# Kernel optimization log

Hardware: AMD Instinct MI355X
Metric: run time of the kernel (lower is better)

The kernel has to match this reference:

```python
import jax, jax.numpy as jnp
import numpy as np
from jax import lax

KS = 7  # kernel-prediction footprint at 1/4 res
DN = ('NCHW', 'OIHW', 'NCHW')


def _conv(x, W, b):
    y = lax.conv_general_dilated(x, W, (1, 1), 'VALID', dimension_numbers=DN)
    return y + b[None, :, None, None]


def _apply_kernels(kernel, data, ks):
    # kernel: [bs, ks*ks, kh, kw]; data: [bs, 1, h, w]
    kh, kw = kernel.shape[2], kernel.shape[3]
    h, w = data.shape[2], data.shape[3]
    ch = (h - (kh + ks - 1)) // 2
    cw = (w - (kw + ks - 1)) // 2
    if ch > 0:
        data = data[:, :, ch:h - ch, :]
    if cw > 0:
        data = data[:, :, :, cw:w - cw]
    # patches: [bs, ks*ks, kh, kw], flat tap index = dy*ks+dx (row-major), same as torch unfold+view
    patches = lax.conv_general_dilated_patches(data, (ks, ks), (1, 1), 'VALID')
    return jnp.sum(kernel * patches, axis=1, keepdims=True)


def _crop_like(a, b):
    dh = (a.shape[2] - b.shape[2]) // 2
    dw = (a.shape[3] - b.shape[3]) // 2
    if dh > 0 or dw > 0:
        a = a[:, :, dh:a.shape[2] - dh, dw:a.shape[3] - dw]
    return a


def _unroll(buf):
    # [bs,4,h,w] quarter-res -> [bs,1,2h,2w] full-res (channel c=2p+q -> offset (p,q))
    bs, _, h, w = buf.shape
    return buf.reshape(bs, 2, 2, h, w).transpose(0, 3, 1, 4, 2).reshape(bs, 1, 2 * h, 2 * w)


def reference(mosaic, W0, b0, W1, b1, W2, b2, W3, b3, W4, b4):
    gray = mosaic.sum(axis=1)  # [bs,H,W]
    # GRBG 2x2 phase extraction, matching torch unfold(2,2,2).unfold(1,2,2).permute(0,3,4,1,2)
    g0 = gray[:, 0::2, 0::2][:, None]
    b_ = gray[:, 1::2, 0::2][:, None]
    r = gray[:, 0::2, 1::2][:, None]
    g1 = gray[:, 1::2, 1::2][:, None]
    x = jnp.concatenate([g0, b_, r, g1], axis=1)  # [bs,4,h,w]

    # ConvChain: 5 valid 3x3 convs, relu on all but last (linear output)
    for (W, bb) in ((W0, b0), (W1, b1), (W2, b2), (W3, b3)):
        x = jax.nn.relu(_conv(x, W, bb))
    kernels = _conv(x, W4, b4)  # [bs, 10*KS*KS, kh, kw]

    k2 = KS * KS
    idx = 0

    reds = [r]
    for _ in range(3):
        k = jax.nn.softmax(kernels[:, idx:idx + k2], axis=1)
        idx += k2
        reds.append(_apply_kernels(k, r, KS))
    reds[0] = _crop_like(reds[0], reds[1])
    red = _unroll(jnp.concatenate([reds[1], reds[0], reds[2], reds[3]], axis=1))

    blues = [b_]
    for _ in range(3):
        k = jax.nn.softmax(kernels[:, idx:idx + k2], axis=1)
        idx += k2
        blues.append(_apply_kernels(k, b_, KS))
    blues[0] = _crop_like(blues[0], blues[1])
    blue = _unroll(jnp.concatenate([blues[1], blues[2], blues[0], blues[3]], axis=1))

    greens = [g0, g1]
    for _ in range(2):
        k = jax.nn.softmax(kernels[:, idx:idx + 2 * k2], axis=1)
        idx += 2 * k2
        greens.append(_apply_kernels(k[:, :k2], g0, KS) + _apply_kernels(k[:, k2:], g1, KS))
    greens[0] = _crop_like(greens[0], greens[2])
    greens[1] = _crop_like(greens[1], greens[2])
    green = _unroll(jnp.concatenate([greens[0], greens[2], greens[3], greens[1]], axis=1))

    return jnp.concatenate([red, green, blue], axis=1)  # [bs,3,2*kh,2*kw]


def setup_inputs() -> dict:
    key = jax.random.key(0)
    ks = jax.random.split(key, 6)
    bs, H, W = 2, 768, 768
    mosaic = jax.random.uniform(ks[0], (bs, 3, H, W), dtype=jnp.float32)

    def w(k, o, i):
        return jax.random.normal(k, (o, i, 3, 3), jnp.float32) * (1.0 / np.sqrt(i * 9))

    z = lambda n: jnp.zeros((n,), jnp.float32)
    return {
        'mosaic': mosaic,
        'W0': w(ks[1], 64, 4), 'b0': z(64),
        'W1': w(ks[2], 64, 64), 'b1': z(64),
        'W2': w(ks[3], 64, 64), 'b2': z(64),
        'W3': w(ks[4], 64, 64), 'b3': z(64),
        'W4': w(ks[5], 490, 64), 'b4': z(490),
    }
```

## Files before the change

### kernel.cpp

```cpp
#include <hip/hip_runtime.h>
#include <hip/hip_bf16.h>
#include <math.h>


typedef __attribute__((ext_vector_type(8))) short short8;
typedef __attribute__((ext_vector_type(4))) short short4v;
typedef __attribute__((ext_vector_type(4))) float f32x4;

static __device__ __forceinline__ short f2bf(float v) {
    __bf16 h = (__bf16)v;
    return __builtin_bit_cast(short, h);
}

__global__ __launch_bounds__(256) void split_k(const float* __restrict__ mosaic,
                                               float* __restrict__ x0) {
    int idx = blockIdx.x * 256 + threadIdx.x;
    const int total = 2 * 4 * 384 * 384;
    if (idx >= total) return;
    int x = idx % 384;
    int t = idx / 384;
    int y = t % 384;  t /= 384;
    int c = t % 4;
    int b = t / 4;
    int Y = 2 * y + ((c == 1 || c == 3) ? 1 : 0);
    int X = 2 * x + ((c == 2 || c == 3) ? 1 : 0);
    const float* mb = mosaic + (size_t)b * 3 * 768 * 768;
    float g = mb[Y * 768 + X] + mb[768 * 768 + Y * 768 + X] + mb[2 * 768 * 768 + Y * 768 + X];
    x0[idx] = g;
}

__global__ __launch_bounds__(256) void repack_k(const float* __restrict__ W,
                                                short* __restrict__ dst) {
    int idx = blockIdx.x * 256 + threadIdx.x;
    if (idx >= 9 * 64 * 64) return;
    int ic = idx % 64;
    int t2 = idx / 64;
    int oc = t2 % 64;
    int t  = t2 / 64;
    dst[idx] = f2bf(W[((size_t)oc * 64 + ic) * 9 + t]);
}

__global__ __launch_bounds__(256) void repack4_k(const float* __restrict__ W4,
                                                 const float* __restrict__ b4,
                                                 short* __restrict__ Wq,
                                                 float* __restrict__ bq) {
    int idx = blockIdx.x * 256 + threadIdx.x;
    if (idx < 9 * 640 * 64) {
        int ic  = idx % 64;
        int t2  = idx / 64;
        int ocn = t2 % 640;
        int tap = t2 / 640;
        int k  = ocn >> 6;
        int ql = ocn & 63;
        float v = (ql < 49) ? W4[((size_t)(49 * k + ql) * 64 + ic) * 9 + tap] : 0.f;
        Wq[idx] = f2bf(v);
    }
    if (idx < 640) {
        int k = idx >> 6, ql = idx & 63;
        bq[idx] = (ql < 49) ? b4[49 * k + ql] : 0.f;
    }
}

__global__ __launch_bounds__(256) void conv0_k(const float* __restrict__ x0f,
                                               const float* __restrict__ W0,
                                               const float* __restrict__ b0,
                                               short* __restrict__ out) {
    __shared__ float w[64 * 36];
    __shared__ float bb[64];
    for (int e = threadIdx.x; e < 64 * 36; e += 256) w[e] = W0[e];
    if (threadIdx.x < 64) bb[threadIdx.x] = b0[threadIdx.x];
    __syncthreads();
    int idx = blockIdx.x * 256 + threadIdx.x;
    if (idx >= 2 * 382 * 382) return;
    int x = idx % 382;
    int t = idx / 382;
    int y = t % 382;
    int b = t / 382;
    const float* base = x0f + (size_t)b * 4 * 384 * 384;
    float in[4][9];
#pragma unroll
    for (int ic = 0; ic < 4; ++ic)
#pragma unroll
        for (int ky = 0; ky < 3; ++ky)
#pragma unroll
            for (int kx = 0; kx < 3; ++kx)
                in[ic][ky * 3 + kx] = base[ic * 384 * 384 + (y + ky) * 384 + (x + kx)];
    short* op = out + (((size_t)b * 382 + y) * 382 + x) * 64;
    float accs[8];
    for (int og = 0; og < 8; ++og) {
#pragma unroll
        for (int oo = 0; oo < 8; ++oo) {
            int oc = og * 8 + oo;
            float acc = bb[oc];
            const float* wp = w + oc * 36;
#pragma unroll
            for (int ic = 0; ic < 4; ++ic)
#pragma unroll
                for (int e = 0; e < 9; ++e)
                    acc = fmaf(in[ic][e], wp[ic * 9 + e], acc);
            accs[oo] = fmaxf(acc, 0.f);
        }
        short8 pk;
#pragma unroll
        for (int oo = 0; oo < 8; ++oo) pk[oo] = f2bf(accs[oo]);
        *(short8*)(op + og * 8) = pk;
    }
}

__global__ __launch_bounds__(256) void convmfma_k(
    const short* __restrict__ act, int Hin, int Win,
    const short* __restrict__ Wq, const float* __restrict__ bias,
    short* __restrict__ out) {
    const int Wout = Win - 2;
    const int b   = blockIdx.z;
    const int y   = blockIdx.y;
    const int x0  = blockIdx.x * 64;
    const int tid  = threadIdx.x;
    const int wave = tid >> 6;
    const int lane = tid & 63;
    const int wr = wave >> 1, wc = wave & 1;

    __shared__ __align__(16) short At[64][72];
    __shared__ __align__(16) short Bt[64][72];

    const int srow = tid >> 2;
    const int sq   = tid & 3;

    short8 ra0, ra1, rb0, rb1;
    auto loadA = [&](int tap) {
        const short* p = Wq + ((size_t)tap * 64 + srow) * 64 + sq * 16;
        ra0 = *(const short8*)p;
        ra1 = *(const short8*)(p + 8);
    };
    auto loadB = [&](int tap) {
        int ky = tap / 3, kx = tap % 3;
        int xe = x0 + srow;
        if (xe > Wout - 1) xe = Wout - 1;
        xe += kx;
        const short* p = act + (((size_t)b * Hin + (y + ky)) * (size_t)Win + xe) * 64 + sq * 16;
        rb0 = *(const short8*)p;
        rb1 = *(const short8*)(p + 8);
    };

    f32x4 acc[2][2] = {};
    loadA(0);
    loadB(0);
#pragma unroll 1
    for (int tap = 0; tap < 9; ++tap) {
        if (tap) __syncthreads();
        *(short8*)&At[srow][sq * 16]     = ra0;
        *(short8*)&At[srow][sq * 16 + 8] = ra1;
        *(short8*)&Bt[srow][sq * 16]     = rb0;
        *(short8*)&Bt[srow][sq * 16 + 8] = rb1;
        __syncthreads();
        if (tap < 8) { loadA(tap + 1); loadB(tap + 1); }
        short8 af[2][2], bf[2][2];
#pragma unroll
        for (int kk = 0; kk < 2; ++kk) {
            int ic = kk * 32 + (lane >> 4) * 8;
#pragma unroll
            for (int m = 0; m < 2; ++m)
                af[kk][m] = *(const short8*)&At[wr * 32 + m * 16 + (lane & 15)][ic];
#pragma unroll
            for (int n = 0; n < 2; ++n)
                bf[kk][n] = *(const short8*)&Bt[wc * 32 + n * 16 + (lane & 15)][ic];
        }
#pragma unroll
        for (int kk = 0; kk < 2; ++kk)
#pragma unroll
            for (int m = 0; m < 2; ++m)
#pragma unroll
                for (int n = 0; n < 2; ++n)
                    acc[m][n] = __builtin_amdgcn_mfma_f32_16x16x32_bf16(
                        af[kk][m], bf[kk][n], acc[m][n], 0, 0, 0);
    }

#pragma unroll
    for (int m = 0; m < 2; ++m) {
        int ocb = wr * 32 + m * 16 + (lane >> 4) * 4;
#pragma unroll
        for (int n = 0; n < 2; ++n) {
            int x = x0 + wc * 32 + n * 16 + (lane & 15);
            if (x >= Wout) continue;
            size_t off = (((size_t)b * Wout + y) * Wout + x) * 64 + ocb;
            short4v pk;
#pragma unroll
            for (int r = 0; r < 4; ++r)
                pk[r] = f2bf(fmaxf(acc[m][n][r] + bias[ocb + r], 0.f));
            *(short4v*)(out + off) = pk;
        }
    }
}

__global__ __launch_bounds__(256) void conv4epi_k(
    const short* __restrict__ act,
    const short* __restrict__ Wq,
    const float* __restrict__ bias,
    const float* __restrict__ x0f,
    float* __restrict__ out) {
    const int Hin = 376, Win = 376, Wout = 374;
    const int z5 = blockIdx.z;
    const int b = z5 / 5;
    const int z = z5 % 5;
    const int y = blockIdx.y;
    const int x0c = blockIdx.x * 64;
    const int tid = threadIdx.x;
    const int wave = tid >> 6;
    const int lane = tid & 63;
    const int wr = wave >> 1, wc = wave & 1;
    const int l15 = lane & 15, l4 = lane >> 4;

    __shared__ __align__(16) short At[128][72];
    __shared__ __align__(16) short Bt[64][72];
    __shared__ float smM[2][64], smD[2][64], smN[2][64];

    const int arow = tid >> 1;
    const int ah   = tid & 1;
    const int brow = tid >> 2;
    const int bq   = tid & 3;

    short8 ra0, ra1, ra2, ra3, rb0, rb1;
    auto loadA = [&](int tap) {
        const short* p = Wq + ((size_t)tap * 640 + z * 128 + arow) * 64 + ah * 32;
        ra0 = *(const short8*)p;
        ra1 = *(const short8*)(p + 8);
        ra2 = *(const short8*)(p + 16);
        ra3 = *(const short8*)(p + 24);
    };
    auto loadB = [&](int tap) {
        int ky = tap / 3, kx = tap % 3;
        int xe = x0c + brow;
        if (xe > Wout - 1) xe = Wout - 1;
        xe += kx;
        const short* p = act + (((size_t)b * Hin + (y + ky)) * (size_t)Win + xe) * 64 + bq * 16;
        rb0 = *(const short8*)p;
        rb1 = *(const short8*)(p + 8);
    };

    f32x4 acc[4][2] = {};
    loadA(0);
    loadB(0);
#pragma unroll 1
    for (int tap = 0; tap < 9; ++tap) {
        if (tap) __syncthreads();
        *(short8*)&At[arow][ah * 32]      = ra0;
        *(short8*)&At[arow][ah * 32 + 8]  = ra1;
        *(short8*)&At[arow][ah * 32 + 16] = ra2;
        *(short8*)&At[arow][ah * 32 + 24] = ra3;
        *(short8*)&Bt[brow][bq * 16]      = rb0;
        *(short8*)&Bt[brow][bq * 16 + 8]  = rb1;
        __syncthreads();
        if (tap < 8) { loadA(tap + 1); loadB(tap + 1); }
        short8 af[2][4], bf[2][2];
#pragma unroll
        for (int kk = 0; kk < 2; ++kk) {
            int ic = kk * 32 + l4 * 8;
#pragma unroll
            for (int m = 0; m < 4; ++m)
                af[kk][m] = *(const short8*)&At[wr * 64 + m * 16 + l15][ic];
#pragma unroll
            for (int n = 0; n < 2; ++n)
                bf[kk][n] = *(const short8*)&Bt[wc * 32 + n * 16 + l15][ic];
        }
#pragma unroll
        for (int kk = 0; kk < 2; ++kk)
#pragma unroll
            for (int m = 0; m < 4; ++m)
#pragma unroll
                for (int n = 0; n < 2; ++n)
                    acc[m][n] = __builtin_amdgcn_mfma_f32_16x16x32_bf16(
                        af[kk][m], bf[kk][n], acc[m][n], 0, 0, 0);
    }

    const float* pb = x0f + (size_t)b * 4 * 384 * 384;
    int pidx;
    switch (z) {
        case 0: pidx = 2; break;
        case 1: pidx = wr ? 1 : 2; break;
        case 2: pidx = 1; break;
        default: pidx = wr ? 3 : 0; break;
    }
    const float* plane = pb + (size_t)pidx * 384 * 384;

    float bv[4][4];
#pragma unroll
    for (int m = 0; m < 4; ++m)
#pragma unroll
        for (int r = 0; r < 4; ++r)
            bv[m][r] = bias[z * 128 + wr * 64 + m * 16 + l4 * 4 + r];

#pragma unroll
    for (int n = 0; n < 2; ++n) {
        const int xn = x0c + wc * 32 + n * 16 + l15;
        const int xg = (xn < Wout) ? xn : (Wout - 1);
        float mx = -1e30f;
#pragma unroll
        for (int m = 0; m < 4; ++m)
#pragma unroll
            for (int r = 0; r < 4; ++r) {
                int q = m * 16 + l4 * 4 + r;
                if (q < 49) mx = fmaxf(mx, acc[m][n][r] + bv[m][r]);
            }
        mx = fmaxf(mx, __shfl_xor(mx, 16));
        mx = fmaxf(mx, __shfl_xor(mx, 32));
        float den = 0.f, num = 0.f;
#pragma unroll
        for (int m = 0; m < 4; ++m)
#pragma unroll
            for (int r = 0; r < 4; ++r) {
                int q = m * 16 + l4 * 4 + r;
                if (q < 49) {
                    float e = __expf(acc[m][n][r] + bv[m][r] - mx);
                    den += e;
                    float g = plane[(y + 2 + q / 7) * 384 + (xg + 2 + q % 7)];
                    num = fmaf(e, g, num);
                }
            }
        den += __shfl_xor(den, 16);  den += __shfl_xor(den, 32);
        num += __shfl_xor(num, 16);  num += __shfl_xor(num, 32);
        if (l4 == 0) {
            int p = wc * 32 + n * 16 + l15;
            smM[wr][p] = mx;
            smD[wr][p] = den;
            smN[wr][p] = num;
        }
    }
    __syncthreads();

    if (z < 3) {
        if (tid < 128) {
            int sub = tid >> 6, p = tid & 63;
            int x = x0c + p;
            if (x < Wout) {
                float val = smN[sub][p] / smD[sub][p];
                int t = z * 2 + sub;
                int color = (t < 3) ? 0 : 2;
                int oy, ox;
                switch (t) {
                    case 0: oy = 0; ox = 0; break;
                    case 1: oy = 1; ox = 0; break;
                    case 2: oy = 1; ox = 1; break;
                    case 3: oy = 0; ox = 0; break;
                    case 4: oy = 0; ox = 1; break;
                    default: oy = 1; ox = 1; break;
                }
                out[(((size_t)b * 3 + color) * 748 + 2 * y + oy) * 748 + 2 * x + ox] = val;
            }
        }
    } else {
        if (tid < 64) {
            int p = tid, x = x0c + p;
            if (x < Wout) {
                float m0 = smM[0][p], m1 = smM[1][p];
                float M = fmaxf(m0, m1);
                float s0 = __expf(m0 - M), s1 = __expf(m1 - M);
                float val = (smN[0][p] * s0 + smN[1][p] * s1) /
                            (smD[0][p] * s0 + smD[1][p] * s1);
                int oy = (z == 3) ? 0 : 1;
                int ox = (z == 3) ? 1 : 0;
                out[(((size_t)b * 3 + 1) * 748 + 2 * y + oy) * 748 + 2 * x + ox] = val;
            }
        }
    }
}

__global__ __launch_bounds__(256) void raw_k(const float* __restrict__ x0f,
                                             float* __restrict__ out) {
    int idx = blockIdx.x * 256 + threadIdx.x;
    if (idx >= 2 * 374 * 374) return;
    int x = idx % 374;
    int t = idx / 374;
    int y = t % 374;
    int b = t / 374;
    const float* pb = x0f + (size_t)b * 4 * 384 * 384;
    float g0v = pb[(y + 5) * 384 + x + 5];
    float blv = pb[384 * 384 + (y + 5) * 384 + x + 5];
    float rrv = pb[2 * 384 * 384 + (y + 5) * 384 + x + 5];
    float g1v = pb[3 * 384 * 384 + (y + 5) * 384 + x + 5];
    float* ob = out + (size_t)b * 3 * 748 * 748;
    ob[((size_t)0 * 748 + 2 * y) * 748 + 2 * x + 1]     = rrv;
    ob[((size_t)2 * 748 + 2 * y + 1) * 748 + 2 * x]     = blv;
    ob[((size_t)1 * 748 + 2 * y) * 748 + 2 * x]         = g0v;
    ob[((size_t)1 * 748 + 2 * y + 1) * 748 + 2 * x + 1] = g1v;
}

extern "C" void kernel_launch(void* const* d_in, const int* in_sizes, int n_in,
                              void* d_out, int out_size, void* d_ws, size_t ws_size,
                              hipStream_t stream) {
    const float* mosaic = (const float*)d_in[0];
    const float* W0 = (const float*)d_in[1];  const float* b0 = (const float*)d_in[2];
    const float* W1 = (const float*)d_in[3];  const float* b1 = (const float*)d_in[4];
    const float* W2 = (const float*)d_in[5];  const float* b2 = (const float*)d_in[6];
    const float* W3 = (const float*)d_in[7];  const float* b3 = (const float*)d_in[8];
    const float* W4 = (const float*)d_in[9];  const float* b4 = (const float*)d_in[10];
    float* out = (float*)d_out;

    char* ws = (char*)d_ws;
    float* x0f    = (float*)ws;  ws += 4718592;
    short* Wq1    = (short*)ws;  ws += 73728;
    short* Wq2    = (short*)ws;  ws += 73728;
    short* Wq3    = (short*)ws;  ws += 73728;
    short* Wq4p   = (short*)ws;  ws += 737280;
    float* bias4p = (float*)ws;  ws += 2560;
    short* bufA   = (short*)ws;  ws += 37356544;
    short* bufB   = (short*)ws;

    split_k<<<(2 * 4 * 384 * 384 + 255) / 256, 256, 0, stream>>>(mosaic, x0f);

    repack_k<<<(9 * 64 * 64 + 255) / 256, 256, 0, stream>>>(W1, Wq1);
    repack_k<<<(9 * 64 * 64 + 255) / 256, 256, 0, stream>>>(W2, Wq2);
    repack_k<<<(9 * 64 * 64 + 255) / 256, 256, 0, stream>>>(W3, Wq3);
    repack4_k<<<(9 * 640 * 64 + 255) / 256, 256, 0, stream>>>(W4, b4, Wq4p, bias4p);

    conv0_k<<<(2 * 382 * 382 + 255) / 256, 256, 0, stream>>>(x0f, W0, b0, bufA);

    convmfma_k<<<dim3(6, 380, 2), 256, 0, stream>>>(bufA, 382, 382, Wq1, b1, bufB);
    convmfma_k<<<dim3(6, 378, 2), 256, 0, stream>>>(bufB, 380, 380, Wq2, b2, bufA);
    convmfma_k<<<dim3(6, 376, 2), 256, 0, stream>>>(bufA, 378, 378, Wq3, b3, bufB);

    conv4epi_k<<<dim3(6, 374, 2 * 5), 256, 0, stream>>>(bufB, Wq4p, bias4p, x0f, out);
    raw_k<<<(2 * 374 * 374 + 255) / 256, 256, 0, stream>>>(x0f, out);
}
```

Before: 511.3 us.

## Unify convs into one templated kernel with async LDS patch staging and direct weight loads

Replaces the per-tap staged conv kernels with one templated kernel. It loads the whole 3x66 input patch into LDS once using global_load_lds, with an XOR swizzle to avoid bank conflicts. Each of the 9 taps then reads shifted slices from that patch, and weight fragments are read directly from global memory instead of being staged through LDS. The block index is remapped across 8 groups (XCD-style), which changes which blocks run together. This removes the per-tap barriers and redundant activation loads, at the cost of larger LDS use and weight reads that depend on cache hits.

```diff
diff --git a/kernel.cpp b/kernel.cpp
--- a/kernel.cpp
+++ b/kernel.cpp
@@ -107,258 +107,188 @@
     }
 }
 
-__global__ __launch_bounds__(256) void convmfma_k(
-    const short* __restrict__ act, int Hin, int Win,
-    const short* __restrict__ Wq, const float* __restrict__ bias,
-    short* __restrict__ out) {
-    const int Wout = Win - 2;
-    const int b   = blockIdx.z;
-    const int y   = blockIdx.y;
-    const int x0  = blockIdx.x * 64;
-    const int tid  = threadIdx.x;
-    const int wave = tid >> 6;
-    const int lane = tid & 63;
-    const int wr = wave >> 1, wc = wave & 1;
-
-    __shared__ __align__(16) short At[64][72];
-    __shared__ __align__(16) short Bt[64][72];
-
-    const int srow = tid >> 2;
-    const int sq   = tid & 3;
-
-    short8 ra0, ra1, rb0, rb1;
-    auto loadA = [&](int tap) {
-        const short* p = Wq + ((size_t)tap * 64 + srow) * 64 + sq * 16;
-        ra0 = *(const short8*)p;
-        ra1 = *(const short8*)(p + 8);
-    };
-    auto loadB = [&](int tap) {
-        int ky = tap / 3, kx = tap % 3;
-        int xe = x0 + srow;
-        if (xe > Wout - 1) xe = Wout - 1;
-        xe += kx;
-        const short* p = act + (((size_t)b * Hin + (y + ky)) * (size_t)Win + xe) * 64 + sq * 16;
-        rb0 = *(const short8*)p;
-        rb1 = *(const short8*)(p + 8);
-    };
-
-    f32x4 acc[2][2] = {};
-    loadA(0);
-    loadB(0);
-#pragma unroll 1
-    for (int tap = 0; tap < 9; ++tap) {
-        if (tap) __syncthreads();
-        *(short8*)&At[srow][sq * 16]     = ra0;
-        *(short8*)&At[srow][sq * 16 + 8] = ra1;
-        *(short8*)&Bt[srow][sq * 16]     = rb0;
-        *(short8*)&Bt[srow][sq * 16 + 8] = rb1;
-        __syncthreads();
-        if (tap < 8) { loadA(tap + 1); loadB(tap + 1); }
-        short8 af[2][2], bf[2][2];
-#pragma unroll
-        for (int kk = 0; kk < 2; ++kk) {
-            int ic = kk * 32 + (lane >> 4) * 8;
-#pragma unroll
-            for (int m = 0; m < 2; ++m)
-                af[kk][m] = *(const short8*)&At[wr * 32 + m * 16 + (lane & 15)][ic];
-#pragma unroll
-            for (int n = 0; n < 2; ++n)
-                bf[kk][n] = *(const short8*)&Bt[wc * 32 + n * 16 + (lane & 15)][ic];
-        }
-#pragma unroll
-        for (int kk = 0; kk < 2; ++kk)
-#pragma unroll
-            for (int m = 0; m < 2; ++m)
-#pragma unroll
-                for (int n = 0; n < 2; ++n)
-                    acc[m][n] = __builtin_amdgcn_mfma_f32_16x16x32_bf16(
-                        af[kk][m], bf[kk][n], acc[m][n], 0, 0, 0);
-    }
-
-#pragma unroll
-    for (int m = 0; m < 2; ++m) {
-        int ocb = wr * 32 + m * 16 + (lane >> 4) * 4;
-#pragma unroll
-        for (int n = 0; n < 2; ++n) {
-            int x = x0 + wc * 32 + n * 16 + (lane & 15);
-            if (x >= Wout) continue;
-            size_t off = (((size_t)b * Wout + y) * Wout + x) * 64 + ocb;
-            short4v pk;
-#pragma unroll
-            for (int r = 0; r < 4; ++r)
-                pk[r] = f2bf(fmaxf(acc[m][n][r] + bias[ocb + r], 0.f));
-            *(short4v*)(out + off) = pk;
-        }
-    }
-}
-
-__global__ __launch_bounds__(256) void conv4epi_k(
+template <int MW, bool EPI>
+__global__ __launch_bounds__(256) void convfused_k(
     const short* __restrict__ act,
+    int Hin, int Hout,
     const short* __restrict__ Wq,
+    int CoutT,
     const float* __restrict__ bias,
+    short* __restrict__ outbf,
     const float* __restrict__ x0f,
     float* __restrict__ out) {
-    const int Hin = 376, Win = 376, Wout = 374;
-    const int z5 = blockIdx.z;
-    const int b = z5 / 5;
-    const int z = z5 % 5;
-    const int y = blockIdx.y;
-    const int x0c = blockIdx.x * 64;
+    const int Win = Hin;
+    const int Wout = Hin - 2;
     const int tid = threadIdx.x;
     const int wave = tid >> 6;
     const int lane = tid & 63;
     const int wr = wave >> 1, wc = wave & 1;
     const int l15 = lane & 15, l4 = lane >> 4;
 
-    __shared__ __align__(16) short At[128][72];
-    __shared__ __align__(16) short Bt[64][72];
-    __shared__ float smM[2][64], smD[2][64], smN[2][64];
-
-    const int arow = tid >> 1;
-    const int ah   = tid & 1;
-    const int brow = tid >> 2;
-    const int bq   = tid & 3;
-
-    short8 ra0, ra1, ra2, ra3, rb0, rb1;
-    auto loadA = [&](int tap) {
-        const short* p = Wq + ((size_t)tap * 640 + z * 128 + arow) * 64 + ah * 32;
-        ra0 = *(const short8*)p;
-        ra1 = *(const short8*)(p + 8);
-        ra2 = *(const short8*)(p + 16);
-        ra3 = *(const short8*)(p + 24);
-    };
-    auto loadB = [&](int tap) {
-        int ky = tap / 3, kx = tap % 3;
-        int xe = x0c + brow;
-        if (xe > Wout - 1) xe = Wout - 1;
-        xe += kx;
-        const short* p = act + (((size_t)b * Hin + (y + ky)) * (size_t)Win + xe) * 64 + bq * 16;
-        rb0 = *(const short8*)p;
-        rb1 = *(const short8*)(p + 8);
-    };
-
-    f32x4 acc[4][2] = {};
-    loadA(0);
-    loadB(0);
-#pragma unroll 1
+    const int q8 = gridDim.x >> 3;
+    const int L = (blockIdx.x & 7) * q8 + (blockIdx.x >> 3);
+    int b, y, x0c, z;
+    if (EPI) {
+        int zx = L % 30; z = zx % 5; x0c = (zx / 5) * 64;
+        int t = L / 30;  y = t % 374; b = t / 374;
+    } else {
+        x0c = (L % 6) * 64;
+        int t = L / 6;   y = t % Hout; b = t / Hout; z = 0;
+    }
+
+    __shared__ __align__(16) short Bt[1792 * 8];
+    for (int i = 0; i < 7; ++i) {
+        int s  = i * 256 + tid;
+        int ss = s < 1584 ? s : 1583;
+        int row = ss >> 3, sl = ss & 7;
+        int ky = row / 66, xl = row % 66;
+        int gx = x0c + xl;
+        if (gx > Win - 1) gx = Win - 1;
+        const short* src = act + (((size_t)b * Hin + (y + ky)) * (size_t)Win + gx) * 64
+                               + ((sl ^ (xl & 7)) << 3);
+        __builtin_amdgcn_global_load_lds((const __attribute__((address_space(1))) void*)src,
+                                         (__attribute__((address_space(3))) void*)((char*)Bt + s * 16),
+                                         16, 0, 0);
+    }
+    __syncthreads();
+
+    const int zrow = EPI ? z * 128 : 0;
+    f32x4 acc[MW][2] = {};
+#pragma unroll
     for (int tap = 0; tap < 9; ++tap) {
-        if (tap) __syncthreads();
-        *(short8*)&At[arow][ah * 32]      = ra0;
-        *(short8*)&At[arow][ah * 32 + 8]  = ra1;
-        *(short8*)&At[arow][ah * 32 + 16] = ra2;
-        *(short8*)&At[arow][ah * 32 + 24] = ra3;
-        *(short8*)&Bt[brow][bq * 16]      = rb0;
-        *(short8*)&Bt[brow][bq * 16 + 8]  = rb1;
-        __syncthreads();
-        if (tap < 8) { loadA(tap + 1); loadB(tap + 1); }
-        short8 af[2][4], bf[2][2];
-#pragma unroll
-        for (int kk = 0; kk < 2; ++kk) {
-            int ic = kk * 32 + l4 * 8;
-#pragma unroll
-            for (int m = 0; m < 4; ++m)
-                af[kk][m] = *(const short8*)&At[wr * 64 + m * 16 + l15][ic];
-#pragma unroll
-            for (int n = 0; n < 2; ++n)
-                bf[kk][n] = *(const short8*)&Bt[wc * 32 + n * 16 + l15][ic];
-        }
+        const int ky = tap / 3, kx = tap % 3;
+        short8 af[2][MW], bf[2][2];
 #pragma unroll
         for (int kk = 0; kk < 2; ++kk)
 #pragma unroll
-            for (int m = 0; m < 4; ++m)
+            for (int m = 0; m < MW; ++m)
+                af[kk][m] = *(const short8*)(Wq +
+                    ((size_t)tap * CoutT + zrow + wr * (MW * 16) + m * 16 + l15) * 64
+                    + kk * 32 + l4 * 8);
+#pragma unroll
+        for (int kk = 0; kk < 2; ++kk)
+#pragma unroll
+            for (int n = 0; n < 2; ++n) {
+                int xl = wc * 32 + n * 16 + l15 + kx;
+                int slot = (kk * 4 + l4) ^ (xl & 7);
+                bf[kk][n] = *(const short8*)&Bt[(((ky * 66 + xl) << 3) + slot) << 3];
+            }
+#pragma unroll
+        for (int kk = 0; kk < 2; ++kk)
+#pragma unroll
+            for (int m = 0; m < MW; ++m)
 #pragma unroll
                 for (int n = 0; n < 2; ++n)
                     acc[m][n] = __builtin_amdgcn_mfma_f32_16x16x32_bf16(
                         af[kk][m], bf[kk][n], acc[m][n], 0, 0, 0);
     }
 
-    const float* pb = x0f + (size_t)b * 4 * 384 * 384;
-    int pidx;
-    switch (z) {
-        case 0: pidx = 2; break;
-        case 1: pidx = wr ? 1 : 2; break;
-        case 2: pidx = 1; break;
-        default: pidx = wr ? 3 : 0; break;
-    }
-    const float* plane = pb + (size_t)pidx * 384 * 384;
-
-    float bv[4][4];
-#pragma unroll
-    for (int m = 0; m < 4; ++m)
-#pragma unroll
-        for (int r = 0; r < 4; ++r)
-            bv[m][r] = bias[z * 128 + wr * 64 + m * 16 + l4 * 4 + r];
-
-#pragma unroll
-    for (int n = 0; n < 2; ++n) {
-        const int xn = x0c + wc * 32 + n * 16 + l15;
-        const int xg = (xn < Wout) ? xn : (Wout - 1);
-        float mx = -1e30f;
-#pragma unroll
-        for (int m = 0; m < 4; ++m)
-#pragma unroll
-            for (int r = 0; r < 4; ++r) {
-                int q = m * 16 + l4 * 4 + r;
-                if (q < 49) mx = fmaxf(mx, acc[m][n][r] + bv[m][r]);
-            }
-        mx = fmaxf(mx, __shfl_xor(mx, 16));
-        mx = fmaxf(mx, __shfl_xor(mx, 32));
-        float den = 0.f, num = 0.f;
-#pragma unroll
-        for (int m = 0; m < 4; ++m)
-#pragma unroll
-            for (int r = 0; r < 4; ++r) {
-                int q = m * 16 + l4 * 4 + r;
-                if (q < 49) {
-                    float e = __expf(acc[m][n][r] + bv[m][r] - mx);
-                    den += e;
-                    float g = plane[(y + 2 + q / 7) * 384 + (xg + 2 + q % 7)];
-                    num = fmaf(e, g, num);
+    if (!EPI) {
+#pragma unroll
+        for (int m = 0; m < MW; ++m) {
+            int ocb = wr * (MW * 16) + m * 16 + l4 * 4;
+#pragma unroll
+            for (int n = 0; n < 2; ++n) {
+                int x = x0c + wc * 32 + n * 16 + l15;
+                if (x >= Wout) continue;
+                size_t off = (((size_t)b * Wout + y) * Wout + x) * 64 + ocb;
+                short4v pk;
+#pragma unroll
+                for (int r = 0; r < 4; ++r)
+                    pk[r] = f2bf(fmaxf(acc[m][n][r] + bias[ocb + r], 0.f));
+                *(short4v*)(outbf + off) = pk;
+            }
+        }
+    } else {
+        __shared__ float smM[2][64], smD[2][64], smN[2][64];
+        const float* pb = x0f + (size_t)b * 4 * 384 * 384;
+        int pidx;
+        switch (z) {
+            case 0: pidx = 2; break;
+            case 1: pidx = wr ? 1 : 2; break;
+            case 2: pidx = 1; break;
+            default: pidx = wr ? 3 : 0; break;
+        }
+        const float* plane = pb + (size_t)pidx * 384 * 384;
+
+        float bv[MW][4];
+#pragma unroll
+        for (int m = 0; m < MW; ++m)
+#pragma unroll
+            for (int r = 0; r < 4; ++r)
+                bv[m][r] = bias[z * 128 + wr * 64 + m * 16 + l4 * 4 + r];
+
+#pragma unroll
+        for (int n = 0; n < 2; ++n) {
+            const int xn = x0c + wc * 32 + n * 16 + l15;
+            const int xg = (xn < 374) ? xn : 373;
+            float mx = -1e30f;
+#pragma unroll
+            for (int m = 0; m < MW; ++m)
+#pragma unroll
+                for (int r = 0; r < 4; ++r) {
+                    int qq = m * 16 + l4 * 4 + r;
+                    if (qq < 49) mx = fmaxf(mx, acc[m][n][r] + bv[m][r]);
                 }
-            }
-        den += __shfl_xor(den, 16);  den += __shfl_xor(den, 32);
-        num += __shfl_xor(num, 16);  num += __shfl_xor(num, 32);
-        if (l4 == 0) {
-            int p = wc * 32 + n * 16 + l15;
-            smM[wr][p] = mx;
-            smD[wr][p] = den;
-            smN[wr][p] = num;
-        }
-    }
-    __syncthreads();
-
-    if (z < 3) {
-        if (tid < 128) {
-            int sub = tid >> 6, p = tid & 63;
-            int x = x0c + p;
-            if (x < Wout) {
-                float val = smN[sub][p] / smD[sub][p];
-                int t = z * 2 + sub;
-                int color = (t < 3) ? 0 : 2;
-                int oy, ox;
-                switch (t) {
-                    case 0: oy = 0; ox = 0; break;
-                    case 1: oy = 1; ox = 0; break;
-                    case 2: oy = 1; ox = 1; break;
-                    case 3: oy = 0; ox = 0; break;
-                    case 4: oy = 0; ox = 1; break;
-                    default: oy = 1; ox = 1; break;
+            mx = fmaxf(mx, __shfl_xor(mx, 16));
+            mx = fmaxf(mx, __shfl_xor(mx, 32));
+            float den = 0.f, num = 0.f;
+#pragma unroll
+            for (int m = 0; m < MW; ++m)
+#pragma unroll
+                for (int r = 0; r < 4; ++r) {
+                    int qq = m * 16 + l4 * 4 + r;
+                    if (qq < 49) {
+                        float e = __expf(acc[m][n][r] + bv[m][r] - mx);
+                        den += e;
+                        float g = plane[(y + 2 + qq / 7) * 384 + (xg + 2 + qq % 7)];
+                        num = fmaf(e, g, num);
+                    }
                 }
-                out[(((size_t)b * 3 + color) * 748 + 2 * y + oy) * 748 + 2 * x + ox] = val;
-            }
-        }
-    } else {
-        if (tid < 64) {
-            int p = tid, x = x0c + p;
-            if (x < Wout) {
-                float m0 = smM[0][p], m1 = smM[1][p];
-                float M = fmaxf(m0, m1);
-                float s0 = __expf(m0 - M), s1 = __expf(m1 - M);
-                float val = (smN[0][p] * s0 + smN[1][p] * s1) /
-                            (smD[0][p] * s0 + smD[1][p] * s1);
-                int oy = (z == 3) ? 0 : 1;
-                int ox = (z == 3) ? 1 : 0;
-                out[(((size_t)b * 3 + 1) * 748 + 2 * y + oy) * 748 + 2 * x + ox] = val;
+            den += __shfl_xor(den, 16);  den += __shfl_xor(den, 32);
+            num += __shfl_xor(num, 16);  num += __shfl_xor(num, 32);
+            if (l4 == 0) {
+                int p = wc * 32 + n * 16 + l15;
+                smM[wr][p] = mx;
+                smD[wr][p] = den;
+                smN[wr][p] = num;
+            }
+        }
+        __syncthreads();
+
+        if (z < 3) {
+            if (tid < 128) {
+                int sub = tid >> 6, p = tid & 63;
+                int x = x0c + p;
+                if (x < 374) {
+                    float val = smN[sub][p] / smD[sub][p];
+                    int t = z * 2 + sub;
+                    int color = (t < 3) ? 0 : 2;
+                    int oy, ox;
+                    switch (t) {
+                        case 0: oy = 0; ox = 0; break;
+                        case 1: oy = 1; ox = 0; break;
+                        case 2: oy = 1; ox = 1; break;
+                        case 3: oy = 0; ox = 0; break;
+                        case 4: oy = 0; ox = 1; break;
+                        default: oy = 1; ox = 1; break;
+                    }
+                    out[(((size_t)b * 3 + color) * 748 + 2 * y + oy) * 748 + 2 * x + ox] = val;
+                }
+            }
+        } else {
+            if (tid < 64) {
+                int p = tid, x = x0c + p;
+                if (x < 374) {
+                    float m0 = smM[0][p], m1 = smM[1][p];
+                    float M = fmaxf(m0, m1);
+                    float s0 = __expf(m0 - M), s1 = __expf(m1 - M);
+                    float val = (smN[0][p] * s0 + smN[1][p] * s1) /
+                                (smD[0][p] * s0 + smD[1][p] * s1);
+                    int oy = (z == 3) ? 0 : 1;
+                    int ox = (z == 3) ? 1 : 0;
+                    out[(((size_t)b * 3 + 1) * 748 + 2 * y + oy) * 748 + 2 * x + ox] = val;
+                }
             }
         }
     }
@@ -414,10 +344,15 @@
 
     conv0_k<<<(2 * 382 * 382 + 255) / 256, 256, 0, stream>>>(x0f, W0, b0, bufA);
 
-    convmfma_k<<<dim3(6, 380, 2), 256, 0, stream>>>(bufA, 382, 382, Wq1, b1, bufB);
-    convmfma_k<<<dim3(6, 378, 2), 256, 0, stream>>>(bufB, 380, 380, Wq2, b2, bufA);
-    convmfma_k<<<dim3(6, 376, 2), 256, 0, stream>>>(bufA, 378, 378, Wq3, b3, bufB);
-
-    conv4epi_k<<<dim3(6, 374, 2 * 5), 256, 0, stream>>>(bufB, Wq4p, bias4p, x0f, out);
+    convfused_k<2, false><<<6 * 380 * 2, 256, 0, stream>>>(
+        bufA, 382, 380, Wq1, 64, b1, bufB, nullptr, nullptr);
+    convfused_k<2, false><<<6 * 378 * 2, 256, 0, stream>>>(
+        bufB, 380, 378, Wq2, 64, b2, bufA, nullptr, nullptr);
+    convfused_k<2, false><<<6 * 376 * 2, 256, 0, stream>>>(
+        bufA, 378, 376, Wq3, 64, b3, bufB, nullptr, nullptr);
+
+    convfused_k<4, true><<<30 * 374 * 2, 256, 0, stream>>>(
+        bufB, 376, 374, Wq4p, 640, bias4p, nullptr, x0f, out);
+
     raw_k<<<(2 * 374 * 374 + 255) / 256, 256, 0, stream>>>(x0f, out);
 }
```

Result: slower. 1.103 ms (+115.7%).
